# Performance work log

Hardware: AMD Instinct MI355X
Metric: run time of the kernel (lower is better)

Reference implementation:

```python
import jax, jax.numpy as jnp
import numpy as np

N_NODES = 100000
N_EDGES = 1600000
C_IN = 64
C_OUT = 64
FILL = 2.0  # improved=True self-loop weight


def setup_inputs() -> dict:
    key = jax.random.key(0)
    k1, k2, k3, k4 = jax.random.split(key, 4)
    x = jax.random.normal(k1, (N_NODES, C_IN), dtype=jnp.float32)
    edge_index = jax.random.randint(k2, (2, N_EDGES), 0, N_NODES, dtype=jnp.int64)
    edge_weight = jax.random.uniform(k3, (N_EDGES,), dtype=jnp.float32)
    W = jax.random.normal(k4, (C_IN, C_OUT), dtype=jnp.float32) / np.sqrt(C_IN)
    b = jnp.zeros((C_OUT,), dtype=jnp.float32)
    return {"x": x, "edge_index": edge_index, "edge_weight": edge_weight, "W": W, "b": b}


def reference(x, edge_index, edge_weight, W, b):
    N = x.shape[0]
    src, dst = edge_index[0], edge_index[1]
    # add self-loops with fill value 2.0 (improved GCN)
    loop = jnp.arange(N)
    src_f = jnp.concatenate([src, loop])
    dst_f = jnp.concatenate([dst, loop])
    w_f = jnp.concatenate([edge_weight, jnp.full((N,), FILL, dtype=x.dtype)])
    # symmetric degree normalization
    deg = jax.ops.segment_sum(w_f, dst_f, num_segments=N)
    dinv = jnp.where(deg > 0, jax.lax.rsqrt(deg), jnp.zeros_like(deg))
    norm = dinv[src_f] * w_f * dinv[dst_f]  # [E+N]
    # linear transform then gather-scale-scatter aggregation
    xw = x @ W  # [N, C_OUT]
    msg = xw[src_f] * norm[:, None]  # [E+N, C_OUT]
    out = jax.ops.segment_sum(msg, dst_f, num_segments=N) + b
    return jnp.tanh(out)
```

## Files before the change

kernel.cpp:

```cpp
#include <hip/hip_runtime.h>
#include <hip/hip_bf16.h>

#define NNODES 100000
#define NEDGES 1600000
#define FILLW 2.0f
#define CAP 64
#define NPART 196
#define PSHIFT 9
#define PNODES 512
#define PCAP 9216
#define EPB 4096
#define NBLKA ((NEDGES + EPB - 1) / EPB)


union PairU { struct { int s; float n; } p; long long ll; };

__global__ void k_partA(const void* ei, const float* __restrict__ w,
                        int* g_cursor, unsigned long long* __restrict__ part) {
  __shared__ int hist[NPART], base[NPART], cur[NPART];
  int t = threadIdx.x;
  for (int i = t; i < NPART; i += 256) { hist[i] = 0; cur[i] = 0; base[i] = 0; }
  __syncthreads();
  long long e0 = (long long)blockIdx.x * EPB;
  long long lim = e0 + EPB < NEDGES ? e0 + EPB : NEDGES;
  long long pe = e0 + t;
  long long pv = ((const long long*)ei)[pe < NEDGES ? pe : 0];
  bool ok = (pv >= 0) && (pv < NNODES);
  bool is64 = (__ballot(ok) == ~0ull);
  for (long long e = e0 + t; e < lim; e += 256) {
    int d = is64 ? (int)((const long long*)ei)[NEDGES + e]
                 : ((const int*)ei)[NEDGES + e];
    atomicAdd(&hist[d >> PSHIFT], 1);
  }
  __syncthreads();
  for (int i = t; i < NPART; i += 256)
    if (hist[i] > 0) base[i] = atomicAdd(&g_cursor[i], hist[i]);
  __syncthreads();
  for (long long e = e0 + t; e < lim; e += 256) {
    int s, d;
    if (is64) {
      s = (int)((const long long*)ei)[e];
      d = (int)((const long long*)ei)[NEDGES + e];
    } else {
      s = ((const int*)ei)[e];
      d = ((const int*)ei)[NEDGES + e];
    }
    float wt = w[e];
    int p = d >> PSHIFT, dl = d & (PNODES - 1);
    int pos = base[p] + atomicAdd(&cur[p], 1);
    if (pos < PCAP) {
      unsigned long long pk =
          ((unsigned long long)__float_as_uint(wt) << 32) |
          ((unsigned long long)(unsigned)dl << 17) | (unsigned)s;
      part[(long long)p * PCAP + pos] = pk;
    }
  }
}

__global__ void k_partB(const unsigned long long* __restrict__ part,
                        const int* __restrict__ g_cursor,
                        long long* __restrict__ bucket,
                        int* __restrict__ cnt, float* __restrict__ dinv) {
  __shared__ int lcnt[PNODES];
  __shared__ float lw[PNODES];
  int p = blockIdx.x, t = threadIdx.x;
  lcnt[t] = 0;
  lw[t] = FILLW;
  __syncthreads();
  int n = min(g_cursor[p], PCAP);
  const unsigned long long* pp = part + (long long)p * PCAP;
  for (int i = t; i < n; i += PNODES) {
    unsigned long long pk = pp[i];
    int s = (int)(pk & 0x1FFFFu);
    int dl = (int)((pk >> 17) & 0x3FFu);
    float wt = __uint_as_float((unsigned)(pk >> 32));
    int pos = atomicAdd(&lcnt[dl], 1);
    if (pos < CAP) {
      PairU u; u.p.s = s; u.p.n = wt;
      bucket[(long long)((p << PSHIFT) + dl) * CAP + pos] = u.ll;
    }
    atomicAdd(&lw[dl], wt);
  }
  __syncthreads();
  int node = (p << PSHIFT) + t;
  if (node < NNODES) {
    cnt[node] = min(lcnt[t], CAP);
    float s = lw[t];
    dinv[node] = s > 0.f ? rsqrtf(s) : 0.f;
  }
}

__global__ void k_gemm(const float* __restrict__ x, const float* __restrict__ W,
                       float* __restrict__ xw) {
  __shared__ float Ws[64 * 64];
  __shared__ float Xs[64 * 64];
  int t = threadIdx.x;
  const float4* W4 = (const float4*)W;
  float4* Ws4w = (float4*)Ws;
#pragma unroll
  for (int i = 0; i < 4; ++i) Ws4w[t + i * 256] = W4[t + i * 256];
  long long row0 = (long long)blockIdx.x * 64;
  const float4* x4 = (const float4*)x;
#pragma unroll
  for (int i = 0; i < 4; ++i) {
    int idx = t + i * 256;
    int r = idx >> 4;
    int kq = idx & 15;
    long long row = row0 + r;
    float4 v = {0.f, 0.f, 0.f, 0.f};
    if (row < NNODES) v = x4[row * 16 + kq];
    int swz = r ^ (kq << 2);
#pragma unroll
    for (int j = 0; j < 4; ++j) {
      float e = (j == 0) ? v.x : (j == 1) ? v.y : (j == 2) ? v.z : v.w;
      Xs[(4 * kq + j) * 64 + swz] = e;
    }
  }
  __syncthreads();
  int cg = t & 15;
  int rg = t >> 4;
  const float4* Xs4 = (const float4*)Xs;
  const float4* Ws4 = (const float4*)Ws;
  float acc[4][4];
#pragma unroll
  for (int i = 0; i < 4; ++i)
#pragma unroll
    for (int j = 0; j < 4; ++j) acc[i][j] = 0.f;
#pragma unroll 8
  for (int k = 0; k < 64; ++k) {
    float4 xv = Xs4[(k << 4) + (rg ^ (k >> 2))];
    float4 wv = Ws4[(k << 4) + cg];
#define FMA4(i, xe)                                                            \
    acc[i][0] = fmaf(xe, wv.x, acc[i][0]);                                     \
    acc[i][1] = fmaf(xe, wv.y, acc[i][1]);                                     \
    acc[i][2] = fmaf(xe, wv.z, acc[i][2]);                                     \
    acc[i][3] = fmaf(xe, wv.w, acc[i][3]);
    FMA4(0, xv.x) FMA4(1, xv.y) FMA4(2, xv.z) FMA4(3, xv.w)
#undef FMA4
  }
  float4* xw4 = (float4*)xw;
#pragma unroll
  for (int i = 0; i < 4; ++i) {
    long long row = row0 + 4 * rg + i;
    if (row < NNODES) {
      float4 o = {acc[i][0], acc[i][1], acc[i][2], acc[i][3]};
      xw4[row * 16 + cg] = o;
    }
  }
}

__global__ void k_agg(const long long* __restrict__ bucket,
                      const int* __restrict__ cnt,
                      const float* __restrict__ dinv,
                      const float* __restrict__ xw,
                      const float* __restrict__ b, float* __restrict__ out) {
  int t = blockIdx.x * blockDim.x + threadIdx.x;
  int d = t >> 6;
  if (d >= NNODES) return;
  int lane = t & 63;
  int sub = lane >> 4;
  int l16 = lane & 15;
  const float4* xw4 = (const float4*)xw;
  float di = dinv[d];
  float4 acc = {0.f, 0.f, 0.f, 0.f};
  if (sub == 0) {
    float4 r = xw4[(long long)d * 16 + l16];
    float c = 2.f * di * di;
    acc.x = r.x * c; acc.y = r.y * c; acc.z = r.z * c; acc.w = r.w * c;
  }
  int n = min(cnt[d], CAP);
  const long long* bp = bucket + (long long)d * CAP;
  int i = sub;
  for (; i + 4 < n; i += 8) {
    PairU u0, u1;
    u0.ll = bp[i];
    u1.ll = bp[i + 4];
    float n0 = dinv[u0.p.s] * u0.p.n * di;
    float n1 = dinv[u1.p.s] * u1.p.n * di;
    float4 r0 = xw4[(long long)u0.p.s * 16 + l16];
    float4 r1 = xw4[(long long)u1.p.s * 16 + l16];
    acc.x = fmaf(r0.x, n0, acc.x); acc.y = fmaf(r0.y, n0, acc.y);
    acc.z = fmaf(r0.z, n0, acc.z); acc.w = fmaf(r0.w, n0, acc.w);
    acc.x = fmaf(r1.x, n1, acc.x); acc.y = fmaf(r1.y, n1, acc.y);
    acc.z = fmaf(r1.z, n1, acc.z); acc.w = fmaf(r1.w, n1, acc.w);
  }
  if (i < n) {
    PairU u; u.ll = bp[i];
    float nm = dinv[u.p.s] * u.p.n * di;
    float4 r = xw4[(long long)u.p.s * 16 + l16];
    acc.x = fmaf(r.x, nm, acc.x); acc.y = fmaf(r.y, nm, acc.y);
    acc.z = fmaf(r.z, nm, acc.z); acc.w = fmaf(r.w, nm, acc.w);
  }
  acc.x += __shfl_xor(acc.x, 16); acc.y += __shfl_xor(acc.y, 16);
  acc.z += __shfl_xor(acc.z, 16); acc.w += __shfl_xor(acc.w, 16);
  acc.x += __shfl_xor(acc.x, 32); acc.y += __shfl_xor(acc.y, 32);
  acc.z += __shfl_xor(acc.z, 32); acc.w += __shfl_xor(acc.w, 32);
  if (sub == 0) {
    float4 bv = ((const float4*)b)[l16];
    float4 o;
    o.x = tanhf(acc.x + bv.x); o.y = tanhf(acc.y + bv.y);
    o.z = tanhf(acc.z + bv.z); o.w = tanhf(acc.w + bv.w);
    ((float4*)out)[(long long)d * 16 + l16] = o;
  }
}

extern "C" void kernel_launch(void* const* d_in, const int* in_sizes, int n_in,
                              void* d_out, int out_size, void* d_ws, size_t ws_size,
                              hipStream_t stream) {
  const float* x = (const float*)d_in[0];
  const void* ei = d_in[1];
  const float* w = (const float*)d_in[2];
  const float* W = (const float*)d_in[3];
  const float* b = (const float*)d_in[4];
  float* out = (float*)d_out;
  float* wsf = (float*)d_ws;
  int* wsi = (int*)d_ws;

  int* g_cursor = wsi;
  int* cnt = wsi + 256;
  float* dinv = wsf + 100352;
  unsigned long long* part = (unsigned long long*)(wsf + 200704);
  float* xw = wsf + 200704;
  long long* bucket = (long long*)(wsf + 6600704);

  hipMemsetAsync(g_cursor, 0, NPART * sizeof(int), stream);
  k_partA<<<NBLKA, 256, 0, stream>>>(ei, w, g_cursor, part);
  k_partB<<<NPART, PNODES, 0, stream>>>(part, g_cursor, bucket, cnt, dinv);
  k_gemm<<<(NNODES + 63) / 64, 256, 0, stream>>>(x, W, xw);
  k_agg<<<(NNODES * 64 + 255) / 256, 256, 0, stream>>>(bucket, cnt, dinv, xw, b, out);
}
```

Before: 135.7 us.

## Restructure aggregation to lane-per-channel with cooperative edge load and shuffle broadcast

The aggregation kernel now assigns one of the 64 channels to each lane instead of splitting edges across four 16-lane groups with float4 loads. Each lane loads one bucket entry and computes its norm, and the entries are broadcast with __shfl so every edge's dinv lookup happens once per wave. This removes the cross-group shuffle reduction and the redundant per-group bucket and dinv loads. In exchange, gathers become 4-byte per lane rather than float4 and there are many more shuffles. The loop is also serial over edges, unrolled by four, which may expose more gather latency.

```diff
diff --git a/kernel.cpp b/kernel.cpp
--- a/kernel.cpp
+++ b/kernel.cpp
@@ -158,50 +158,35 @@
   int d = t >> 6;
   if (d >= NNODES) return;
   int lane = t & 63;
-  int sub = lane >> 4;
-  int l16 = lane & 15;
-  const float4* xw4 = (const float4*)xw;
   float di = dinv[d];
-  float4 acc = {0.f, 0.f, 0.f, 0.f};
-  if (sub == 0) {
-    float4 r = xw4[(long long)d * 16 + l16];
-    float c = 2.f * di * di;
-    acc.x = r.x * c; acc.y = r.y * c; acc.z = r.z * c; acc.w = r.w * c;
-  }
   int n = min(cnt[d], CAP);
-  const long long* bp = bucket + (long long)d * CAP;
-  int i = sub;
-  for (; i + 4 < n; i += 8) {
-    PairU u0, u1;
-    u0.ll = bp[i];
-    u1.ll = bp[i + 4];
-    float n0 = dinv[u0.p.s] * u0.p.n * di;
-    float n1 = dinv[u1.p.s] * u1.p.n * di;
-    float4 r0 = xw4[(long long)u0.p.s * 16 + l16];
-    float4 r1 = xw4[(long long)u1.p.s * 16 + l16];
-    acc.x = fmaf(r0.x, n0, acc.x); acc.y = fmaf(r0.y, n0, acc.y);
-    acc.z = fmaf(r0.z, n0, acc.z); acc.w = fmaf(r0.w, n0, acc.w);
-    acc.x = fmaf(r1.x, n1, acc.x); acc.y = fmaf(r1.y, n1, acc.y);
-    acc.z = fmaf(r1.z, n1, acc.z); acc.w = fmaf(r1.w, n1, acc.w);
-  }
-  if (i < n) {
-    PairU u; u.ll = bp[i];
-    float nm = dinv[u.p.s] * u.p.n * di;
-    float4 r = xw4[(long long)u.p.s * 16 + l16];
-    acc.x = fmaf(r.x, nm, acc.x); acc.y = fmaf(r.y, nm, acc.y);
-    acc.z = fmaf(r.z, nm, acc.z); acc.w = fmaf(r.w, nm, acc.w);
-  }
-  acc.x += __shfl_xor(acc.x, 16); acc.y += __shfl_xor(acc.y, 16);
-  acc.z += __shfl_xor(acc.z, 16); acc.w += __shfl_xor(acc.w, 16);
-  acc.x += __shfl_xor(acc.x, 32); acc.y += __shfl_xor(acc.y, 32);
-  acc.z += __shfl_xor(acc.z, 32); acc.w += __shfl_xor(acc.w, 32);
-  if (sub == 0) {
-    float4 bv = ((const float4*)b)[l16];
-    float4 o;
-    o.x = tanhf(acc.x + bv.x); o.y = tanhf(acc.y + bv.y);
-    o.z = tanhf(acc.z + bv.z); o.w = tanhf(acc.w + bv.w);
-    ((float4*)out)[(long long)d * 16 + l16] = o;
-  }
+  PairU u;
+  u.ll = bucket[(long long)d * CAP + lane];
+  bool valid = lane < n;
+  int sl = valid ? u.p.s : 0;
+  float nl = valid ? dinv[sl] * u.p.n * di : 0.f;
+  float acc = xw[(long long)d * 64 + lane] * (2.0f * di * di);
+  int e = 0;
+  for (; e + 3 < n; e += 4) {
+    int s0 = __shfl(sl, e + 0), s1 = __shfl(sl, e + 1);
+    int s2 = __shfl(sl, e + 2), s3 = __shfl(sl, e + 3);
+    float n0 = __shfl(nl, e + 0), n1 = __shfl(nl, e + 1);
+    float n2 = __shfl(nl, e + 2), n3 = __shfl(nl, e + 3);
+    float v0 = xw[(long long)s0 * 64 + lane];
+    float v1 = xw[(long long)s1 * 64 + lane];
+    float v2 = xw[(long long)s2 * 64 + lane];
+    float v3 = xw[(long long)s3 * 64 + lane];
+    acc = fmaf(v0, n0, acc);
+    acc = fmaf(v1, n1, acc);
+    acc = fmaf(v2, n2, acc);
+    acc = fmaf(v3, n3, acc);
+  }
+  for (; e < n; ++e) {
+    int s0 = __shfl(sl, e);
+    float n0 = __shfl(nl, e);
+    acc = fmaf(xw[(long long)s0 * 64 + lane], n0, acc);
+  }
+  out[(long long)d * 64 + lane] = tanhf(acc + b[lane]);
 }
 
 extern "C" void kernel_launch(void* const* d_in, const int* in_sizes, int n_in,
```

New measurement: 138.7 us. +2.2%, slower.
